# Kernel optimization log

Hardware: AMD Instinct MI355X
Metric: run time of the kernel (lower is better)

Reference implementation:

```python
import jax, jax.numpy as jnp
import numpy as np

N, E, D = 100000, 1000000, 128  # nodes, edges, feature dim (in=hidden=out)
BN_EPS = 1e-5


def setup_inputs() -> dict:
    key = jax.random.key(0)
    ks = jax.random.split(key, 6)
    inp = {
        "x": jax.random.normal(ks[0], (N, D), dtype=jnp.float32),
        "edge_src": jax.random.randint(ks[1], (E,), 0, N),
        "edge_dst": jax.random.randint(ks[2], (E,), 0, N),
    }
    # GraphConv weights (xavier-ish) and biases for 3 layers
    for i in range(3):
        inp[f"W{i}"] = jax.random.normal(ks[3 + i], (D, D), dtype=jnp.float32) * np.float32(1.0 / np.sqrt(D))
        inp[f"b{i}"] = jnp.zeros((D,), dtype=jnp.float32)
    # BatchNorm (eval mode) params/buffers for the 2 inter-layer BNs
    for i in range(2):
        inp[f"bn_gamma{i}"] = jnp.ones((D,), dtype=jnp.float32)
        inp[f"bn_beta{i}"] = jnp.zeros((D,), dtype=jnp.float32)
        inp[f"bn_mean{i}"] = jnp.zeros((D,), dtype=jnp.float32)
        inp[f"bn_var{i}"] = jnp.ones((D,), dtype=jnp.float32)
    return inp


def _gcn_forward(x, edge_src, edge_dst, Ws, bs, bns):
    n = x.shape[0]
    ones = jnp.ones((edge_src.shape[0],), x.dtype)
    # DGL GraphConv norm='both': D_out^{-1/2} on source, D_in^{-1/2} on dest, degrees clamped to >=1
    deg_out = jnp.clip(jax.ops.segment_sum(ones, edge_src, num_segments=n), 1.0)
    deg_in = jnp.clip(jax.ops.segment_sum(ones, edge_dst, num_segments=n), 1.0)
    norm_src = deg_out ** -0.5
    norm_dst = deg_in ** -0.5
    h = x
    L = len(Ws)
    for i in range(L):
        hs = (h * norm_src[:, None]) @ Ws[i]                     # [N, D] dense transform first
        agg = jax.ops.segment_sum(hs[edge_src], edge_dst, num_segments=n)  # SpMM: gather + scatter-add
        h = agg * norm_dst[:, None] + bs[i]
        if i < L - 1:  # BN (eval) + activation between layers; dropout=0 -> no-op
            g, bta, m, v = bns[i]
            h = (h - m) * jax.lax.rsqrt(v + BN_EPS) * g + bta
            h = jax.nn.relu(h)
    return h


def reference(x, edge_src, edge_dst, W0, b0, W1, b1, W2, b2,
              bn_gamma0, bn_beta0, bn_mean0, bn_var0,
              bn_gamma1, bn_beta1, bn_mean1, bn_var1):
    Ws = (W0, W1, W2)
    bs = (b0, b1, b2)
    bns = ((bn_gamma0, bn_beta0, bn_mean0, bn_var0),
           (bn_gamma1, bn_beta1, bn_mean1, bn_var1))
    return _gcn_forward(x, edge_src, edge_dst, Ws, bs, bns)
```

## Files before the change

kernel.cpp:

```cpp
#include <hip/hip_runtime.h>
#include <hip/hip_fp16.h>
#include <math.h>

#define D 128
#define NSL 32
#define PBU 25088

typedef _Float16 half8 __attribute__((ext_vector_type(8)));
typedef float f32x4 __attribute__((ext_vector_type(4)));

__device__ inline uint pack_f16x2(float a, float b) {
  __half2 h = __floats2half2_rn(a, b);
  return *reinterpret_cast<uint*>(&h);
}
__device__ inline float2 unpack_f16x2(uint p) {
  __half2 h = *reinterpret_cast<__half2*>(&p);
  return __half22float2(h);
}
__device__ inline uint mdiv40(uint x, uint M) {
  return (uint)(((unsigned long long)x * M) >> 40);
}


__global__ __launch_bounds__(1024) void k_build1(const int* __restrict__ esrc,
                                                 const int* __restrict__ edst,
                                                 const float* __restrict__ W0,
                                                 const float* __restrict__ W1,
                                                 const float* __restrict__ W2,
                                                 const float* __restrict__ b0,
                                                 const float* __restrict__ b1,
                                                 const float* __restrict__ b2,
                                                 const float* __restrict__ g0,
                                                 const float* __restrict__ be0,
                                                 const float* __restrict__ mu0,
                                                 const float* __restrict__ vr0,
                                                 const float* __restrict__ g1,
                                                 const float* __restrict__ be1,
                                                 const float* __restrict__ mu1,
                                                 const float* __restrict__ vr1,
                                                 uint* __restrict__ pd,
                                                 uint* __restrict__ ps,
                                                 uchar* __restrict__ rank8,
                                                 ushort* __restrict__ Wt,
                                                 float* __restrict__ CA,
                                                 float* __restrict__ CB,
                                                 int E, int SB) {
  __shared__ uint h[PBU];
  const int b = blockIdx.x;
  const int t = threadIdx.x;
  if (b < 32) {
    for (int j = t; j < PBU; j += 1024) h[j] = 0u;
    __syncthreads();
    const int i0 = b * SB, i1 = min(i0 + SB, E);
    for (int i = i0 + t; i < i1; i += 1024) {
      const int d = edst[i];
      const uint sh = (uint)(d & 3) * 8u;
      const uint old = atomicAdd(&h[d >> 2], 1u << sh);
      rank8[i] = (uchar)((old >> sh) & 0xffu);
    }
    __syncthreads();
    uint* p = pd + (size_t)b * PBU;
    for (int j = t; j < PBU; j += 1024) p[j] = h[j];
  } else if (b < 64) {
    const int sl = b - 32;
    for (int j = t; j < PBU; j += 1024) h[j] = 0u;
    __syncthreads();
    const int i0 = sl * SB, i1 = min(i0 + SB, E);
    for (int i = i0 + t; i < i1; i += 1024) {
      const int s = esrc[i];
      atomicAdd(&h[s >> 2], 1u << ((uint)(s & 3) * 8u));
    }
    __syncthreads();
    uint* p = ps + (size_t)sl * PBU;
    for (int j = t; j < PBU; j += 1024) p[j] = h[j];
  } else if (b < 112) {
    const int li = (b - 64) * 1024 + t;
    const int l = li >> 14;
    const int i = li & 16383;
    const int n = i >> 7, k = i & 127;
    const float* W = (l == 0) ? W0 : ((l == 1) ? W1 : W2);
    Wt[li] = __half_as_ushort(__float2half_rn(W[k * D + n]));
  } else if (t < D) {
    const int c = t;
    float A0 = g0[c] * rsqrtf(vr0[c] + 1e-5f);
    CA[c] = A0;
    CB[c] = (b0[c] - mu0[c]) * A0 + be0[c];
    float A1 = g1[c] * rsqrtf(vr1[c] + 1e-5f);
    CA[D + c] = A1;
    CB[D + c] = (b1[c] - mu1[c]) * A1 + be1[c];
    CA[2 * D + c] = 1.f;
    CB[2 * D + c] = b2[c];
  }
}


__global__ __launch_bounds__(256) void k_build2s(uint* __restrict__ pd,
                                                 const uint* __restrict__ ps,
                                                 int* __restrict__ totd,
                                                 float* __restrict__ ns,
                                                 float* __restrict__ nd,
                                                 int* __restrict__ csum,
                                                 int* __restrict__ rofs,
                                                 int* __restrict__ ticket,
                                                 int N, int nch) {
  __shared__ int sd[256];
  __shared__ int lastf;
  const int t = threadIdx.x;
  const int j = blockIdx.x * 256 + t;
  const int n0 = j * 4;
  uint r0 = 0, r1 = 0, r2 = 0, r3 = 0;
  uint s0 = 0, s1 = 0, s2 = 0, s3 = 0;
#pragma unroll
  for (int sl = 0; sl < NSL; ++sl) {
    const uint v = pd[(size_t)sl * PBU + j];
    pd[(size_t)sl * PBU + j] = r0 | (r1 << 8) | (r2 << 16) | (r3 << 24);
    r0 += v & 0xffu; r1 += (v >> 8) & 0xffu; r2 += (v >> 16) & 0xffu; r3 += (v >> 24) & 0xffu;
    const uint w = ps[(size_t)sl * PBU + j];
    s0 += w & 0xffu; s1 += (w >> 8) & 0xffu; s2 += (w >> 16) & 0xffu; s3 += (w >> 24) & 0xffu;
  }
  const uint rr[4] = {r0, r1, r2, r3};
  const uint ss[4] = {s0, s1, s2, s3};
  int tot = 0;
#pragma unroll
  for (int k = 0; k < 4; ++k) {
    if (n0 + k < N) {
      totd[n0 + k] = (int)rr[k];
      nd[n0 + k] = rsqrtf((float)max(rr[k], 1u));
      ns[n0 + k] = rsqrtf((float)max(ss[k], 1u));
      tot += (int)rr[k];
    }
  }
  sd[t] = tot; __syncthreads();
  for (int off = 128; off > 0; off >>= 1) {
    if (t < off) sd[t] += sd[t + off];
    __syncthreads();
  }
  if (t == 0) {
    csum[blockIdx.x] = sd[0];
    __threadfence();
    lastf = (atomicAdd(ticket, 1) == nch - 1) ? 1 : 0;
  }
  __syncthreads();
  if (lastf && t < 64) {
    __threadfence();
    int run = 0;
    for (int b0 = 0; b0 < nch; b0 += 64) {
      const int idx = b0 + t;
      int v = (idx < nch) ? __hip_atomic_load(&csum[idx], __ATOMIC_RELAXED,
                                              __HIP_MEMORY_SCOPE_AGENT) : 0;
      int sc = v;
#pragma unroll
      for (int off = 1; off < 64; off <<= 1) {
        int u = __shfl_up(sc, off);
        if (t >= off) sc += u;
      }
      if (idx < nch) csum[idx] = run + sc - v;
      run += __shfl(sc, 63);
    }
    if (t == 0) rofs[N] = run;
  }
}


__global__ __launch_bounds__(256) void k_scan_final(const int* __restrict__ totd,
                                                    const int* __restrict__ csum,
                                                    int* __restrict__ rofs, int n) {
  __shared__ int sd[256];
  const int b = blockIdx.x, t = threadIdx.x;
  const int base = b * 1024 + t * 4;
  int v[4]; int s = 0;
#pragma unroll
  for (int i = 0; i < 4; ++i) { v[i] = (base + i < n) ? totd[base + i] : 0; s += v[i]; }
  sd[t] = s; __syncthreads();
  for (int off = 1; off < 256; off <<= 1) {
    int x = (t >= off) ? sd[t - off] : 0;
    __syncthreads();
    sd[t] += x;
    __syncthreads();
  }
  int o = sd[t] - s + csum[b];
#pragma unroll
  for (int i = 0; i < 4; ++i) {
    if (base + i < n) { rofs[base + i] = o; o += v[i]; }
  }
}


__global__ __launch_bounds__(256) void k_sg(const float* __restrict__ X,
                                            const ushort* __restrict__ Wt,
                                            const float* __restrict__ ns,
                                            ushort* __restrict__ out,
                                            const int* __restrict__ esrc,
                                            const int* __restrict__ edst,
                                            const uchar* __restrict__ rank8,
                                            const uint* __restrict__ pd,
                                            const int* __restrict__ rofs,
                                            int* __restrict__ csr,
                                            int M, int E, uint Msb, int GB) {
  if ((int)blockIdx.x >= GB) {
    const int i = ((int)blockIdx.x - GB) * 256 + threadIdx.x;
    if (i < E) {
      const int d = edst[i];
      const uint sl = mdiv40((uint)i, Msb);
      const uint pk = pd[(size_t)sl * PBU + (d >> 2)];
      const uint pfx = (pk >> ((uint)(d & 3) * 8u)) & 0xffu;
      csr[rofs[d] + (int)pfx + (int)rank8[i]] = esrc[i];
    }
    return;
  }
  const int lane = threadIdx.x & 63;
  const int wv = threadIdx.x >> 6;
  const int m0 = (blockIdx.x * 4 + wv) * 32;
  if (m0 >= M) return;
  const int lr = lane & 15;
  const int kg = (lane >> 4) * 8;

  half8 hf[2][4];
  const half8 hz = {};
#pragma unroll
  for (int mt = 0; mt < 2; ++mt) {
    const int row = m0 + mt * 16 + lr;
    if (row < M) {
      const float s = ns[row];
#pragma unroll
      for (int kt = 0; kt < 4; ++kt) {
        const float4 a = *reinterpret_cast<const float4*>(X + (size_t)row * D + kt * 32 + kg);
        const float4 b = *reinterpret_cast<const float4*>(X + (size_t)row * D + kt * 32 + kg + 4);
        half8 hv;
        hv[0] = (_Float16)(a.x * s); hv[1] = (_Float16)(a.y * s);
        hv[2] = (_Float16)(a.z * s); hv[3] = (_Float16)(a.w * s);
        hv[4] = (_Float16)(b.x * s); hv[5] = (_Float16)(b.y * s);
        hv[6] = (_Float16)(b.z * s); hv[7] = (_Float16)(b.w * s);
        hf[mt][kt] = hv;
      }
    } else {
#pragma unroll
      for (int kt = 0; kt < 4; ++kt) hf[mt][kt] = hz;
    }
  }

  f32x4 acc[8][2];
#pragma unroll
  for (int nt = 0; nt < 8; ++nt) { acc[nt][0] = (f32x4)(0.f); acc[nt][1] = (f32x4)(0.f); }

#pragma unroll
  for (int nt = 0; nt < 8; ++nt) {
    const ushort* wb = Wt + (size_t)(nt * 16 + lr) * D + kg;
#pragma unroll
    for (int kt = 0; kt < 4; ++kt) {
      half8 wf = *reinterpret_cast<const half8*>(wb + kt * 32);
      acc[nt][0] = __builtin_amdgcn_mfma_f32_16x16x32_f16(wf, hf[0][kt], acc[nt][0], 0, 0, 0);
      acc[nt][1] = __builtin_amdgcn_mfma_f32_16x16x32_f16(wf, hf[1][kt], acc[nt][1], 0, 0, 0);
    }
  }

  const int mo = lane & 15;
  const int no = (lane >> 4) * 4;
#pragma unroll
  for (int mt = 0; mt < 2; ++mt) {
    const int row = m0 + mt * 16 + mo;
    if (row < M) {
#pragma unroll
      for (int nt = 0; nt < 8; ++nt) {
        uint2 u;
        u.x = pack_f16x2(acc[nt][mt][0], acc[nt][mt][1]);
        u.y = pack_f16x2(acc[nt][mt][2], acc[nt][mt][3]);
        *reinterpret_cast<uint2*>(out + (size_t)row * D + nt * 16 + no) = u;
      }
    }
  }
}


__global__ __launch_bounds__(256) void k_gemm16(const ushort* __restrict__ A,
                                                const ushort* __restrict__ Wt,
                                                ushort* __restrict__ out, int M) {
  const int lane = threadIdx.x & 63;
  const int wv = threadIdx.x >> 6;
  const int m0 = (blockIdx.x * 4 + wv) * 32;
  if (m0 >= M) return;
  const int lr = lane & 15;
  const int kg = (lane >> 4) * 8;

  half8 hf[2][4];
  const half8 hz = {};
#pragma unroll
  for (int mt = 0; mt < 2; ++mt) {
    const int row = m0 + mt * 16 + lr;
    const bool ok = row < M;
#pragma unroll
    for (int kt = 0; kt < 4; ++kt)
      hf[mt][kt] = ok ? *reinterpret_cast<const half8*>(A + (size_t)row * D + kt * 32 + kg)
                      : hz;
  }

  f32x4 acc[8][2];
#pragma unroll
  for (int nt = 0; nt < 8; ++nt) { acc[nt][0] = (f32x4)(0.f); acc[nt][1] = (f32x4)(0.f); }

#pragma unroll
  for (int nt = 0; nt < 8; ++nt) {
    const ushort* wb = Wt + (size_t)(nt * 16 + lr) * D + kg;
#pragma unroll
    for (int kt = 0; kt < 4; ++kt) {
      half8 wf = *reinterpret_cast<const half8*>(wb + kt * 32);
      acc[nt][0] = __builtin_amdgcn_mfma_f32_16x16x32_f16(wf, hf[0][kt], acc[nt][0], 0, 0, 0);
      acc[nt][1] = __builtin_amdgcn_mfma_f32_16x16x32_f16(wf, hf[1][kt], acc[nt][1], 0, 0, 0);
    }
  }

  const int mo = lane & 15;
  const int no = (lane >> 4) * 4;
#pragma unroll
  for (int mt = 0; mt < 2; ++mt) {
    const int row = m0 + mt * 16 + mo;
    if (row < M) {
#pragma unroll
      for (int nt = 0; nt < 8; ++nt) {
        uint2 u;
        u.x = pack_f16x2(acc[nt][mt][0], acc[nt][mt][1]);
        u.y = pack_f16x2(acc[nt][mt][2], acc[nt][mt][3]);
        *reinterpret_cast<uint2*>(out + (size_t)row * D + nt * 16 + no) = u;
      }
    }
  }
}


__global__ __launch_bounds__(256) void k_spmm16(const uint* __restrict__ hs,
                                                const int* __restrict__ csr,
                                                const int* __restrict__ rofs,
                                                const float* __restrict__ nd,
                                                const float* __restrict__ ns,
                                                const float* __restrict__ CA,
                                                const float* __restrict__ CB,
                                                float* __restrict__ outf,
                                                uint* __restrict__ hnext,
                                                int N, int last) {
  const int t = threadIdx.x;
  const int lane = t & 63;
  const int c16 = lane & 15;
  const int gb = lane & ~15;
  const int d = blockIdx.x * 16 + (t >> 4);
  if (d >= N) return;
  const int beg = rofs[d], end = rofs[d + 1];

  float acc[8];
#pragma unroll
  for (int j = 0; j < 8; ++j) acc[j] = 0.f;

  for (int base = beg; base < end; base += 16) {
    const int len = min(16, end - base);
    const int idx = csr[min(base + c16, end - 1)];
#pragma unroll 1
    for (int j = 0; j < len; j += 4) {
      const int l1 = min(j + 1, len - 1), l2 = min(j + 2, len - 1), l3 = min(j + 3, len - 1);
      const int s0 = __shfl(idx, gb + j);
      const int s1 = __shfl(idx, gb + l1);
      const int s2 = __shfl(idx, gb + l2);
      const int s3 = __shfl(idx, gb + l3);
      const float w1 = (j + 1 < len) ? 1.f : 0.f;
      const float w2 = (j + 2 < len) ? 1.f : 0.f;
      const float w3 = (j + 3 < len) ? 1.f : 0.f;
      const uint4 v0 = *reinterpret_cast<const uint4*>(hs + (size_t)s0 * 64 + c16 * 4);
      const uint4 v1 = *reinterpret_cast<const uint4*>(hs + (size_t)s1 * 64 + c16 * 4);
      const uint4 v2 = *reinterpret_cast<const uint4*>(hs + (size_t)s2 * 64 + c16 * 4);
      const uint4 v3 = *reinterpret_cast<const uint4*>(hs + (size_t)s3 * 64 + c16 * 4);
#pragma unroll
      for (int q = 0; q < 4; ++q) {
        const uint u0 = (&v0.x)[q], u1 = (&v1.x)[q], u2 = (&v2.x)[q], u3 = (&v3.x)[q];
        const float2 a0 = unpack_f16x2(u0);
        const float2 a1 = unpack_f16x2(u1);
        const float2 a2 = unpack_f16x2(u2);
        const float2 a3 = unpack_f16x2(u3);
        acc[q * 2]     += a0.x;
        acc[q * 2 + 1] += a0.y;
        acc[q * 2]     = fmaf(a1.x, w1, acc[q * 2]);
        acc[q * 2 + 1] = fmaf(a1.y, w1, acc[q * 2 + 1]);
        acc[q * 2]     = fmaf(a2.x, w2, acc[q * 2]);
        acc[q * 2 + 1] = fmaf(a2.y, w2, acc[q * 2 + 1]);
        acc[q * 2]     = fmaf(a3.x, w3, acc[q * 2]);
        acc[q * 2 + 1] = fmaf(a3.y, w3, acc[q * 2 + 1]);
      }
    }
  }

  const float ndv = nd[d];
  const float4 ca0 = *reinterpret_cast<const float4*>(CA + c16 * 8);
  const float4 ca1 = *reinterpret_cast<const float4*>(CA + c16 * 8 + 4);
  const float4 cb0 = *reinterpret_cast<const float4*>(CB + c16 * 8);
  const float4 cb1 = *reinterpret_cast<const float4*>(CB + c16 * 8 + 4);
  float r[8];
  r[0] = acc[0] * ndv * ca0.x + cb0.x;
  r[1] = acc[1] * ndv * ca0.y + cb0.y;
  r[2] = acc[2] * ndv * ca0.z + cb0.z;
  r[3] = acc[3] * ndv * ca0.w + cb0.w;
  r[4] = acc[4] * ndv * ca1.x + cb1.x;
  r[5] = acc[5] * ndv * ca1.y + cb1.y;
  r[6] = acc[6] * ndv * ca1.z + cb1.z;
  r[7] = acc[7] * ndv * ca1.w + cb1.w;
  if (!last) {
    const float s = ns[d];
#pragma unroll
    for (int j = 0; j < 8; ++j) r[j] = fmaxf(r[j], 0.f) * s;
    uint4 u;
    u.x = pack_f16x2(r[0], r[1]);
    u.y = pack_f16x2(r[2], r[3]);
    u.z = pack_f16x2(r[4], r[5]);
    u.w = pack_f16x2(r[6], r[7]);
    *reinterpret_cast<uint4*>(hnext + (size_t)d * 64 + c16 * 4) = u;
  } else {
    float4 o0 = make_float4(r[0], r[1], r[2], r[3]);
    float4 o1 = make_float4(r[4], r[5], r[6], r[7]);
    *reinterpret_cast<float4*>(outf + (size_t)d * D + c16 * 8) = o0;
    *reinterpret_cast<float4*>(outf + (size_t)d * D + c16 * 8 + 4) = o1;
  }
}


extern "C" void kernel_launch(void* const* d_in, const int* in_sizes, int n_in,
                              void* d_out, int out_size, void* d_ws, size_t ws_size,
                              hipStream_t stream) {
  const float* x = (const float*)d_in[0];
  const int* esrc = (const int*)d_in[1];
  const int* edst = (const int*)d_in[2];
  const float* W0 = (const float*)d_in[3];
  const float* b0 = (const float*)d_in[4];
  const float* W1 = (const float*)d_in[5];
  const float* b1 = (const float*)d_in[6];
  const float* W2 = (const float*)d_in[7];
  const float* b2 = (const float*)d_in[8];
  const float* g0 = (const float*)d_in[9];
  const float* be0 = (const float*)d_in[10];
  const float* m0 = (const float*)d_in[11];
  const float* v0 = (const float*)d_in[12];
  const float* g1 = (const float*)d_in[13];
  const float* be1 = (const float*)d_in[14];
  const float* m1 = (const float*)d_in[15];
  const float* v1 = (const float*)d_in[16];
  const int N = in_sizes[0] / D;
  const int E = in_sizes[1];

  const int SB = (E + NSL - 1) / NSL;
  const uint Msb = (uint)(((1ULL << 40) + (unsigned long long)SB - 1) / (unsigned long long)SB);

  char* p = (char*)d_ws;
  auto carve = [&](size_t bytes) {
    char* r = p;
    p += (bytes + 255) & ~(size_t)255;
    return (void*)r;
  };
  uint* hs16 = (uint*)carve((size_t)N * 64 * 4);
  ushort* Wt = (ushort*)carve((size_t)3 * D * D * 2);
  float* CA = (float*)carve((size_t)3 * D * 4);
  float* CB = (float*)carve((size_t)3 * D * 4);
  float* ns = (float*)carve((size_t)N * 4);
  float* nd = (float*)carve((size_t)N * 4);
  uint* pd = (uint*)carve((size_t)NSL * PBU * 4);
  uint* ps = (uint*)carve((size_t)NSL * PBU * 4);
  uchar* rank8 = (uchar*)carve((size_t)E);
  int* totd = (int*)carve((size_t)N * 4);
  int* rofs = (int*)carve((size_t)(N + 1) * 4);
  const int nch = (N + 1023) / 1024;
  int* csum = (int*)carve((size_t)nch * 4);
  int* ticket = (int*)carve(256);
  int* csr = (int*)carve((size_t)E * 4);
  uint* bufA = (uint*)d_out;

  hipMemsetAsync(ticket, 0, 4, stream);
  k_build1<<<113, 1024, 0, stream>>>(esrc, edst, W0, W1, W2, b0, b1, b2,
                                     g0, be0, m0, v0, g1, be1, m1, v1,
                                     pd, ps, rank8, Wt, CA, CB, E, SB);
  k_build2s<<<nch, 256, 0, stream>>>(pd, ps, totd, ns, nd, csum, rofs, ticket, N, nch);
  k_scan_final<<<nch, 256, 0, stream>>>(totd, csum, rofs, N);

  const int gb = (N + 127) / 128;
  const int sb = (N + 15) / 16;
  const int scb = (E + 255) / 256;
  k_sg<<<gb + scb, 256, 0, stream>>>(x, Wt, ns, (ushort*)hs16, esrc, edst, rank8, pd, rofs,
                                     csr, N, E, Msb, gb);
  k_spmm16<<<sb, 256, 0, stream>>>(hs16, csr, rofs, nd, ns, CA, CB, nullptr, bufA, N, 0);
  k_gemm16<<<gb, 256, 0, stream>>>((const ushort*)bufA, Wt + 16384, (ushort*)hs16, N);
  k_spmm16<<<sb, 256, 0, stream>>>(hs16, csr, rofs, nd, ns, CA + D, CB + D, nullptr, bufA, N, 0);
  k_gemm16<<<gb, 256, 0, stream>>>((const ushort*)bufA, Wt + 32768, (ushort*)hs16, N);
  k_spmm16<<<sb, 256, 0, stream>>>(hs16, csr, rofs, nd, ns, CA + 2 * D, CB + 2 * D,
                                   (float*)d_out, nullptr, N, 1);
}
```

Baseline: 251.7 us.

## Fuse SpMM aggregation with next-layer GEMM through LDS tile

```diff
diff --git a/kernel.cpp b/kernel.cpp
--- a/kernel.cpp
+++ b/kernel.cpp
@@ -272,56 +272,126 @@
 }
 
 
-__global__ __launch_bounds__(256) void k_gemm16(const ushort* __restrict__ A,
-                                                const ushort* __restrict__ Wt,
-                                                ushort* __restrict__ out, int M) {
-  const int lane = threadIdx.x & 63;
-  const int wv = threadIdx.x >> 6;
-  const int m0 = (blockIdx.x * 4 + wv) * 32;
-  if (m0 >= M) return;
+__global__ __launch_bounds__(256) void k_spgm(const uint* __restrict__ hs,
+                                              const int* __restrict__ csr,
+                                              const int* __restrict__ rofs,
+                                              const float* __restrict__ nd,
+                                              const float* __restrict__ ns,
+                                              const float* __restrict__ CA,
+                                              const float* __restrict__ CB,
+                                              const ushort* __restrict__ Wt,
+                                              ushort* __restrict__ out, int N) {
+  __shared__ ushort A[128 * 136];
+  const int t = threadIdx.x;
+  const int lane = t & 63;
+  const int c16 = lane & 15;
+  const int gb = lane & ~15;
+  const int g = t >> 4;
+  const int rbase = blockIdx.x * 128;
+
+#pragma unroll 1
+  for (int r = 0; r < 8; ++r) {
+    const int rl = g + 16 * r;
+    const int d = rbase + rl;
+    uint4 uo = make_uint4(0u, 0u, 0u, 0u);
+    if (d < N) {
+      const int beg = rofs[d], end = rofs[d + 1];
+      float acc[8];
+#pragma unroll
+      for (int j = 0; j < 8; ++j) acc[j] = 0.f;
+      for (int eb = beg; eb < end; eb += 16) {
+        const int len = min(16, end - eb);
+        const int idx = csr[min(eb + c16, end - 1)];
+#pragma unroll 1
+        for (int j = 0; j < len; j += 4) {
+          const int l1 = min(j + 1, len - 1), l2 = min(j + 2, len - 1), l3 = min(j + 3, len - 1);
+          const int s0 = __shfl(idx, gb + j);
+          const int s1 = __shfl(idx, gb + l1);
+          const int s2 = __shfl(idx, gb + l2);
+          const int s3 = __shfl(idx, gb + l3);
+          const float w1 = (j + 1 < len) ? 1.f : 0.f;
+          const float w2 = (j + 2 < len) ? 1.f : 0.f;
+          const float w3 = (j + 3 < len) ? 1.f : 0.f;
+          const uint4 v0 = *reinterpret_cast<const uint4*>(hs + (size_t)s0 * 64 + c16 * 4);
+          const uint4 v1 = *reinterpret_cast<const uint4*>(hs + (size_t)s1 * 64 + c16 * 4);
+          const uint4 v2 = *reinterpret_cast<const uint4*>(hs + (size_t)s2 * 64 + c16 * 4);
+          const uint4 v3 = *reinterpret_cast<const uint4*>(hs + (size_t)s3 * 64 + c16 * 4);
+#pragma unroll
+          for (int q = 0; q < 4; ++q) {
+            const float2 a0 = unpack_f16x2((&v0.x)[q]);
+            const float2 a1 = unpack_f16x2((&v1.x)[q]);
+            const float2 a2 = unpack_f16x2((&v2.x)[q]);
+            const float2 a3 = unpack_f16x2((&v3.x)[q]);
+            acc[q * 2]     += a0.x;
+            acc[q * 2 + 1] += a0.y;
+            acc[q * 2]     = fmaf(a1.x, w1, acc[q * 2]);
+            acc[q * 2 + 1] = fmaf(a1.y, w1, acc[q * 2 + 1]);
+            acc[q * 2]     = fmaf(a2.x, w2, acc[q * 2]);
+            acc[q * 2 + 1] = fmaf(a2.y, w2, acc[q * 2 + 1]);
+            acc[q * 2]     = fmaf(a3.x, w3, acc[q * 2]);
+            acc[q * 2 + 1] = fmaf(a3.y, w3, acc[q * 2 + 1]);
+          }
+        }
+      }
+      const float ndv = nd[d];
+      const float s = ns[d];
+      const float4 ca0 = *reinterpret_cast<const float4*>(CA + c16 * 8);
+      const float4 ca1 = *reinterpret_cast<const float4*>(CA + c16 * 8 + 4);
+      const float4 cb0 = *reinterpret_cast<const float4*>(CB + c16 * 8);
+      const float4 cb1 = *reinterpret_cast<const float4*>(CB + c16 * 8 + 4);
+      float rv[8];
+      rv[0] = acc[0] * ndv * ca0.x + cb0.x;
+      rv[1] = acc[1] * ndv * ca0.y + cb0.y;
+      rv[2] = acc[2] * ndv * ca0.z + cb0.z;
+      rv[3] = acc[3] * ndv * ca0.w + cb0.w;
+      rv[4] = acc[4] * ndv * ca1.x + cb1.x;
+      rv[5] = acc[5] * ndv * ca1.y + cb1.y;
+      rv[6] = acc[6] * ndv * ca1.z + cb1.z;
+      rv[7] = acc[7] * ndv * ca1.w + cb1.w;
+#pragma unroll
+      for (int j = 0; j < 8; ++j) rv[j] = fmaxf(rv[j], 0.f) * s;
+      uo.x = pack_f16x2(rv[0], rv[1]);
+      uo.y = pack_f16x2(rv[2], rv[3]);
+      uo.z = pack_f16x2(rv[4], rv[5]);
+      uo.w = pack_f16x2(rv[6], rv[7]);
+    }
+    *reinterpret_cast<uint4*>(&A[rl * 136 + c16 * 8]) = uo;
+  }
+  __syncthreads();
+
+  const int w = t >> 6;
+  const int m0l = w * 32;
+  const int m0 = rbase + m0l;
+  if (m0 >= N) return;
   const int lr = lane & 15;
   const int kg = (lane >> 4) * 8;
-
   half8 hf[2][4];
-  const half8 hz = {};
 #pragma unroll
   for (int mt = 0; mt < 2; ++mt) {
-    const int row = m0 + mt * 16 + lr;
-    const bool ok = row < M;
+    const int row_l = m0l + mt * 16 + lr;
 #pragma unroll
     for (int kt = 0; kt < 4; ++kt)
-      hf[mt][kt] = ok ? *reinterpret_cast<const half8*>(A + (size_t)row * D + kt * 32 + kg)
-                      : hz;
-  }
-
-  f32x4 acc[8][2];
-#pragma unroll
-  for (int nt = 0; nt < 8; ++nt) { acc[nt][0] = (f32x4)(0.f); acc[nt][1] = (f32x4)(0.f); }
-
+      hf[mt][kt] = *reinterpret_cast<const half8*>(&A[row_l * 136 + kt * 32 + kg]);
+  }
+  const int no = (lane >> 4) * 4;
 #pragma unroll
   for (int nt = 0; nt < 8; ++nt) {
+    f32x4 a0 = (f32x4)(0.f), a1 = (f32x4)(0.f);
     const ushort* wb = Wt + (size_t)(nt * 16 + lr) * D + kg;
 #pragma unroll
     for (int kt = 0; kt < 4; ++kt) {
       half8 wf = *reinterpret_cast<const half8*>(wb + kt * 32);
-      acc[nt][0] = __builtin_amdgcn_mfma_f32_16x16x32_f16(wf, hf[0][kt], acc[nt][0], 0, 0, 0);
-      acc[nt][1] = __builtin_amdgcn_mfma_f32_16x16x32_f16(wf, hf[1][kt], acc[nt][1], 0, 0, 0);
-    }
-  }
-
-  const int mo = lane & 15;
-  const int no = (lane >> 4) * 4;
-#pragma unroll
-  for (int mt = 0; mt < 2; ++mt) {
-    const int row = m0 + mt * 16 + mo;
-    if (row < M) {
-#pragma unroll
-      for (int nt = 0; nt < 8; ++nt) {
-        uint2 u;
-        u.x = pack_f16x2(acc[nt][mt][0], acc[nt][mt][1]);
-        u.y = pack_f16x2(acc[nt][mt][2], acc[nt][mt][3]);
-        *reinterpret_cast<uint2*>(out + (size_t)row * D + nt * 16 + no) = u;
-      }
+      a0 = __builtin_amdgcn_mfma_f32_16x16x32_f16(wf, hf[0][kt], a0, 0, 0, 0);
+      a1 = __builtin_amdgcn_mfma_f32_16x16x32_f16(wf, hf[1][kt], a1, 0, 0, 0);
+    }
+    const int r0 = m0 + lr, r1 = m0 + 16 + lr;
+    if (r0 < N) {
+      uint2 u; u.x = pack_f16x2(a0[0], a0[1]); u.y = pack_f16x2(a0[2], a0[3]);
+      *reinterpret_cast<uint2*>(out + (size_t)r0 * D + nt * 16 + no) = u;
+    }
+    if (r1 < N) {
+      uint2 u; u.x = pack_f16x2(a1[0], a1[1]); u.y = pack_f16x2(a1[2], a1[3]);
+      *reinterpret_cast<uint2*>(out + (size_t)r1 * D + nt * 16 + no) = u;
     }
   }
 }
@@ -331,12 +401,9 @@
                                                 const int* __restrict__ csr,
                                                 const int* __restrict__ rofs,
                                                 const float* __restrict__ nd,
-                                                const float* __restrict__ ns,
                                                 const float* __restrict__ CA,
                                                 const float* __restrict__ CB,
-                                                float* __restrict__ outf,
-                                                uint* __restrict__ hnext,
-                                                int N, int last) {
+                                                float* __restrict__ outf, int N) {
   const int t = threadIdx.x;
   const int lane = t & 63;
   const int c16 = lane & 15;
@@ -368,11 +435,10 @@
       const uint4 v3 = *reinterpret_cast<const uint4*>(hs + (size_t)s3 * 64 + c16 * 4);
 #pragma unroll
       for (int q = 0; q < 4; ++q) {
-        const uint u0 = (&v0.x)[q], u1 = (&v1.x)[q], u2 = (&v2.x)[q], u3 = (&v3.x)[q];
-        const float2 a0 = unpack_f16x2(u0);
-        const float2 a1 = unpack_f16x2(u1);
-        const float2 a2 = unpack_f16x2(u2);
-        const float2 a3 = unpack_f16x2(u3);
+        const float2 a0 = unpack_f16x2((&v0.x)[q]);
+        const float2 a1 = unpack_f16x2((&v1.x)[q]);
+        const float2 a2 = unpack_f16x2((&v2.x)[q]);
+        const float2 a3 = unpack_f16x2((&v3.x)[q]);
         acc[q * 2]     += a0.x;
         acc[q * 2 + 1] += a0.y;
         acc[q * 2]     = fmaf(a1.x, w1, acc[q * 2]);
@@ -390,31 +456,17 @@
   const float4 ca1 = *reinterpret_cast<const float4*>(CA + c16 * 8 + 4);
   const float4 cb0 = *reinterpret_cast<const float4*>(CB + c16 * 8);
   const float4 cb1 = *reinterpret_cast<const float4*>(CB + c16 * 8 + 4);
-  float r[8];
-  r[0] = acc[0] * ndv * ca0.x + cb0.x;
-  r[1] = acc[1] * ndv * ca0.y + cb0.y;
-  r[2] = acc[2] * ndv * ca0.z + cb0.z;
-  r[3] = acc[3] * ndv * ca0.w + cb0.w;
-  r[4] = acc[4] * ndv * ca1.x + cb1.x;
-  r[5] = acc[5] * ndv * ca1.y + cb1.y;
-  r[6] = acc[6] * ndv * ca1.z + cb1.z;
-  r[7] = acc[7] * ndv * ca1.w + cb1.w;
-  if (!last) {
-    const float s = ns[d];
-#pragma unroll
-    for (int j = 0; j < 8; ++j) r[j] = fmaxf(r[j], 0.f) * s;
-    uint4 u;
-    u.x = pack_f16x2(r[0], r[1]);
-    u.y = pack_f16x2(r[2], r[3]);
-    u.z = pack_f16x2(r[4], r[5]);
-    u.w = pack_f16x2(r[6], r[7]);
-    *reinterpret_cast<uint4*>(hnext + (size_t)d * 64 + c16 * 4) = u;
-  } else {
-    float4 o0 = make_float4(r[0], r[1], r[2], r[3]);
-    float4 o1 = make_float4(r[4], r[5], r[6], r[7]);
-    *reinterpret_cast<float4*>(outf + (size_t)d * D + c16 * 8) = o0;
-    *reinterpret_cast<float4*>(outf + (size_t)d * D + c16 * 8 + 4) = o1;
-  }
+  float4 o0, o1;
+  o0.x = acc[0] * ndv * ca0.x + cb0.x;
+  o0.y = acc[1] * ndv * ca0.y + cb0.y;
+  o0.z = acc[2] * ndv * ca0.z + cb0.z;
+  o0.w = acc[3] * ndv * ca0.w + cb0.w;
+  o1.x = acc[4] * ndv * ca1.x + cb1.x;
+  o1.y = acc[5] * ndv * ca1.y + cb1.y;
+  o1.z = acc[6] * ndv * ca1.z + cb1.z;
+  o1.w = acc[7] * ndv * ca1.w + cb1.w;
+  *reinterpret_cast<float4*>(outf + (size_t)d * D + c16 * 8) = o0;
+  *reinterpret_cast<float4*>(outf + (size_t)d * D + c16 * 8 + 4) = o1;
 }
 
 
@@ -465,7 +517,7 @@
   int* csum = (int*)carve((size_t)nch * 4);
   int* ticket = (int*)carve(256);
   int* csr = (int*)carve((size_t)E * 4);
-  uint* bufA = (uint*)d_out;
+  uint* hsOut = (uint*)d_out;
 
   hipMemsetAsync(ticket, 0, 4, stream);
   k_build1<<<113, 1024, 0, stream>>>(esrc, edst, W0, W1, W2, b0, b1, b2,
@@ -475,14 +527,15 @@
   k_scan_final<<<nch, 256, 0, stream>>>(totd, csum, rofs, N);
 
   const int gb = (N + 127) / 128;
+  const int scb = (E + 255) / 256;
+  const int fb = (N + 127) / 128;
   const int sb = (N + 15) / 16;
-  const int scb = (E + 255) / 256;
   k_sg<<<gb + scb, 256, 0, stream>>>(x, Wt, ns, (ushort*)hs16, esrc, edst, rank8, pd, rofs,
                                      csr, N, E, Msb, gb);
-  k_spmm16<<<sb, 256, 0, stream>>>(hs16, csr, rofs, nd, ns, CA, CB, nullptr, bufA, N, 0);
-  k_gemm16<<<gb, 256, 0, stream>>>((const ushort*)bufA, Wt + 16384, (ushort*)hs16, N);
-  k_spmm16<<<sb, 256, 0, stream>>>(hs16, csr, rofs, nd, ns, CA + D, CB + D, nullptr, bufA, N, 0);
-  k_gemm16<<<gb, 256, 0, stream>>>((const ushort*)bufA, Wt + 32768, (ushort*)hs16, N);
-  k_spmm16<<<sb, 256, 0, stream>>>(hs16, csr, rofs, nd, ns, CA + 2 * D, CB + 2 * D,
-                                   (float*)d_out, nullptr, N, 1);
-}
+  k_spgm<<<fb, 256, 0, stream>>>(hs16, csr, rofs, nd, ns, CA, CB, Wt + 16384,
+                                 (ushort*)hsOut, N);
+  k_spgm<<<fb, 256, 0, stream>>>(hsOut, csr, rofs, nd, ns, CA + D, CB + D, Wt + 32768,
+                                 (ushort*)hs16, N);
+  k_spmm16<<<sb, 256, 0, stream>>>(hs16, csr, rofs, nd, CA + 2 * D, CB + 2 * D,
+                                   (float*)d_out, N);
+}
```

Measured after the change: 226.4 us. 1.11x faster.

## Column-chunk the hidden features so each XCD gathers one chunk in SpMM

Applied to the files above, without the earlier changes.

```diff
diff --git a/kernel.cpp b/kernel.cpp
--- a/kernel.cpp
+++ b/kernel.cpp
@@ -265,7 +265,7 @@
         uint2 u;
         u.x = pack_f16x2(acc[nt][mt][0], acc[nt][mt][1]);
         u.y = pack_f16x2(acc[nt][mt][2], acc[nt][mt][3]);
-        *reinterpret_cast<uint2*>(out + (size_t)row * D + nt * 16 + no) = u;
+        *reinterpret_cast<uint2*>(out + ((size_t)nt * M + row) * 16 + no) = u;
       }
     }
   }
@@ -289,9 +289,12 @@
     const int row = m0 + mt * 16 + lr;
     const bool ok = row < M;
 #pragma unroll
-    for (int kt = 0; kt < 4; ++kt)
-      hf[mt][kt] = ok ? *reinterpret_cast<const half8*>(A + (size_t)row * D + kt * 32 + kg)
+    for (int kt = 0; kt < 4; ++kt) {
+      const int off = kt * 32 + kg;
+      const int c = off >> 4, o = off & 15;
+      hf[mt][kt] = ok ? *reinterpret_cast<const half8*>(A + ((size_t)c * M + row) * 16 + o)
                       : hz;
+    }
   }
 
   f32x4 acc[8][2];
@@ -320,100 +323,100 @@
         uint2 u;
         u.x = pack_f16x2(acc[nt][mt][0], acc[nt][mt][1]);
         u.y = pack_f16x2(acc[nt][mt][2], acc[nt][mt][3]);
-        *reinterpret_cast<uint2*>(out + (size_t)row * D + nt * 16 + no) = u;
-      }
-    }
-  }
-}
-
-
-__global__ __launch_bounds__(256) void k_spmm16(const uint* __restrict__ hs,
-                                                const int* __restrict__ csr,
-                                                const int* __restrict__ rofs,
-                                                const float* __restrict__ nd,
-                                                const float* __restrict__ ns,
-                                                const float* __restrict__ CA,
-                                                const float* __restrict__ CB,
-                                                float* __restrict__ outf,
-                                                uint* __restrict__ hnext,
-                                                int N, int last) {
+        *reinterpret_cast<uint2*>(out + ((size_t)nt * M + row) * 16 + no) = u;
+      }
+    }
+  }
+}
+
+
+__global__ __launch_bounds__(256) void k_spmmc(const uint* __restrict__ hs,
+                                               const int* __restrict__ csr,
+                                               const int* __restrict__ rofs,
+                                               const float* __restrict__ nd,
+                                               const float* __restrict__ ns,
+                                               const float* __restrict__ CA,
+                                               const float* __restrict__ CB,
+                                               float* __restrict__ outf,
+                                               uint* __restrict__ hnext,
+                                               int N, int RB, int last) {
   const int t = threadIdx.x;
   const int lane = t & 63;
-  const int c16 = lane & 15;
-  const int gb = lane & ~15;
-  const int d = blockIdx.x * 16 + (t >> 4);
-  if (d >= N) return;
-  const int beg = rofs[d], end = rofs[d + 1];
-
-  float acc[8];
-#pragma unroll
-  for (int j = 0; j < 8; ++j) acc[j] = 0.f;
-
-  for (int base = beg; base < end; base += 16) {
-    const int len = min(16, end - base);
-    const int idx = csr[min(base + c16, end - 1)];
+  const int il = lane & 15;
+  const int slot = il >> 1;
+  const int half = il & 1;
+  const int p = blockIdx.x & 7;
+  const uint* hsC = hs + (size_t)p * N * 8;
+  const int g = t >> 4;
+  const int rb0 = (blockIdx.x >> 3) * (16 * RB);
+
 #pragma unroll 1
-    for (int j = 0; j < len; j += 4) {
-      const int l1 = min(j + 1, len - 1), l2 = min(j + 2, len - 1), l3 = min(j + 3, len - 1);
-      const int s0 = __shfl(idx, gb + j);
-      const int s1 = __shfl(idx, gb + l1);
-      const int s2 = __shfl(idx, gb + l2);
-      const int s3 = __shfl(idx, gb + l3);
-      const float w1 = (j + 1 < len) ? 1.f : 0.f;
-      const float w2 = (j + 2 < len) ? 1.f : 0.f;
-      const float w3 = (j + 3 < len) ? 1.f : 0.f;
-      const uint4 v0 = *reinterpret_cast<const uint4*>(hs + (size_t)s0 * 64 + c16 * 4);
-      const uint4 v1 = *reinterpret_cast<const uint4*>(hs + (size_t)s1 * 64 + c16 * 4);
-      const uint4 v2 = *reinterpret_cast<const uint4*>(hs + (size_t)s2 * 64 + c16 * 4);
-      const uint4 v3 = *reinterpret_cast<const uint4*>(hs + (size_t)s3 * 64 + c16 * 4);
+  for (int r = 0; r < RB; ++r) {
+    const int d = rb0 + r * 16 + g;
+    if (d >= N) break;
+    const int beg = rofs[d], end = rofs[d + 1];
+    float acc[8];
+#pragma unroll
+    for (int j = 0; j < 8; ++j) acc[j] = 0.f;
+#pragma unroll 1
+    for (int eb = beg; eb < end; eb += 16) {
+      const int e0 = eb + slot;
+      const int e1 = eb + slot + 8;
+      const int s0 = csr[min(e0, end - 1)];
+      const int s1 = csr[min(e1, end - 1)];
+      const float w0 = (e0 < end) ? 1.f : 0.f;
+      const float w1 = (e1 < end) ? 1.f : 0.f;
+      const uint4 v0 = *reinterpret_cast<const uint4*>(hsC + (size_t)s0 * 8 + half * 4);
+      const uint4 v1 = *reinterpret_cast<const uint4*>(hsC + (size_t)s1 * 8 + half * 4);
 #pragma unroll
       for (int q = 0; q < 4; ++q) {
-        const uint u0 = (&v0.x)[q], u1 = (&v1.x)[q], u2 = (&v2.x)[q], u3 = (&v3.x)[q];
-        const float2 a0 = unpack_f16x2(u0);
-        const float2 a1 = unpack_f16x2(u1);
-        const float2 a2 = unpack_f16x2(u2);
-        const float2 a3 = unpack_f16x2(u3);
-        acc[q * 2]     += a0.x;
-        acc[q * 2 + 1] += a0.y;
+        const float2 a0 = unpack_f16x2((&v0.x)[q]);
+        const float2 a1 = unpack_f16x2((&v1.x)[q]);
+        acc[q * 2]     = fmaf(a0.x, w0, acc[q * 2]);
+        acc[q * 2 + 1] = fmaf(a0.y, w0, acc[q * 2 + 1]);
         acc[q * 2]     = fmaf(a1.x, w1, acc[q * 2]);
         acc[q * 2 + 1] = fmaf(a1.y, w1, acc[q * 2 + 1]);
-        acc[q * 2]     = fmaf(a2.x, w2, acc[q * 2]);
-        acc[q * 2 + 1] = fmaf(a2.y, w2, acc[q * 2 + 1]);
-        acc[q * 2]     = fmaf(a3.x, w3, acc[q * 2]);
-        acc[q * 2 + 1] = fmaf(a3.y, w3, acc[q * 2 + 1]);
-      }
-    }
-  }
-
-  const float ndv = nd[d];
-  const float4 ca0 = *reinterpret_cast<const float4*>(CA + c16 * 8);
-  const float4 ca1 = *reinterpret_cast<const float4*>(CA + c16 * 8 + 4);
-  const float4 cb0 = *reinterpret_cast<const float4*>(CB + c16 * 8);
-  const float4 cb1 = *reinterpret_cast<const float4*>(CB + c16 * 8 + 4);
-  float r[8];
-  r[0] = acc[0] * ndv * ca0.x + cb0.x;
-  r[1] = acc[1] * ndv * ca0.y + cb0.y;
-  r[2] = acc[2] * ndv * ca0.z + cb0.z;
-  r[3] = acc[3] * ndv * ca0.w + cb0.w;
-  r[4] = acc[4] * ndv * ca1.x + cb1.x;
-  r[5] = acc[5] * ndv * ca1.y + cb1.y;
-  r[6] = acc[6] * ndv * ca1.z + cb1.z;
-  r[7] = acc[7] * ndv * ca1.w + cb1.w;
-  if (!last) {
-    const float s = ns[d];
-#pragma unroll
-    for (int j = 0; j < 8; ++j) r[j] = fmaxf(r[j], 0.f) * s;
-    uint4 u;
-    u.x = pack_f16x2(r[0], r[1]);
-    u.y = pack_f16x2(r[2], r[3]);
-    u.z = pack_f16x2(r[4], r[5]);
-    u.w = pack_f16x2(r[6], r[7]);
-    *reinterpret_cast<uint4*>(hnext + (size_t)d * 64 + c16 * 4) = u;
-  } else {
-    float4 o0 = make_float4(r[0], r[1], r[2], r[3]);
-    float4 o1 = make_float4(r[4], r[5], r[6], r[7]);
-    *reinterpret_cast<float4*>(outf + (size_t)d * D + c16 * 8) = o0;
-    *reinterpret_cast<float4*>(outf + (size_t)d * D + c16 * 8 + 4) = o1;
+      }
+    }
+#pragma unroll
+    for (int j = 0; j < 8; ++j) {
+      acc[j] += __shfl_xor(acc[j], 2);
+      acc[j] += __shfl_xor(acc[j], 4);
+      acc[j] += __shfl_xor(acc[j], 8);
+    }
+    if (il < 2) {
+      const float ndv = nd[d];
+      const int c0 = p * 16 + half * 8;
+      const float4 ca0 = *reinterpret_cast<const float4*>(CA + c0);
+      const float4 ca1 = *reinterpret_cast<const float4*>(CA + c0 + 4);
+      const float4 cb0 = *reinterpret_cast<const float4*>(CB + c0);
+      const float4 cb1 = *reinterpret_cast<const float4*>(CB + c0 + 4);
+      float rv[8];
+      rv[0] = acc[0] * ndv * ca0.x + cb0.x;
+      rv[1] = acc[1] * ndv * ca0.y + cb0.y;
+      rv[2] = acc[2] * ndv * ca0.z + cb0.z;
+      rv[3] = acc[3] * ndv * ca0.w + cb0.w;
+      rv[4] = acc[4] * ndv * ca1.x + cb1.x;
+      rv[5] = acc[5] * ndv * ca1.y + cb1.y;
+      rv[6] = acc[6] * ndv * ca1.z + cb1.z;
+      rv[7] = acc[7] * ndv * ca1.w + cb1.w;
+      if (!last) {
+        const float s = ns[d];
+#pragma unroll
+        for (int j = 0; j < 8; ++j) rv[j] = fmaxf(rv[j], 0.f) * s;
+        uint4 u;
+        u.x = pack_f16x2(rv[0], rv[1]);
+        u.y = pack_f16x2(rv[2], rv[3]);
+        u.z = pack_f16x2(rv[4], rv[5]);
+        u.w = pack_f16x2(rv[6], rv[7]);
+        *reinterpret_cast<uint4*>(hnext + ((size_t)p * N + d) * 8 + half * 4) = u;
+      } else {
+        *reinterpret_cast<float4*>(outf + (size_t)d * D + c0) =
+            make_float4(rv[0], rv[1], rv[2], rv[3]);
+        *reinterpret_cast<float4*>(outf + (size_t)d * D + c0 + 4) =
+            make_float4(rv[4], rv[5], rv[6], rv[7]);
+      }
+    }
   }
 }
 
@@ -450,7 +453,7 @@
     p += (bytes + 255) & ~(size_t)255;
     return (void*)r;
   };
-  uint* hs16 = (uint*)carve((size_t)N * 64 * 4);
+  uint* hsA = (uint*)carve((size_t)N * 64 * 4);
   ushort* Wt = (ushort*)carve((size_t)3 * D * D * 2);
   float* CA = (float*)carve((size_t)3 * D * 4);
   float* CB = (float*)carve((size_t)3 * D * 4);
@@ -465,7 +468,7 @@
   int* csum = (int*)carve((size_t)nch * 4);
   int* ticket = (int*)carve(256);
   int* csr = (int*)carve((size_t)E * 4);
-  uint* bufA = (uint*)d_out;
+  uint* hsB = (uint*)d_out;
 
   hipMemsetAsync(ticket, 0, 4, stream);
   k_build1<<<113, 1024, 0, stream>>>(esrc, edst, W0, W1, W2, b0, b1, b2,
@@ -475,14 +478,16 @@
   k_scan_final<<<nch, 256, 0, stream>>>(totd, csum, rofs, N);
 
   const int gb = (N + 127) / 128;
-  const int sb = (N + 15) / 16;
   const int scb = (E + 255) / 256;
-  k_sg<<<gb + scb, 256, 0, stream>>>(x, Wt, ns, (ushort*)hs16, esrc, edst, rank8, pd, rofs,
+  const int RB = 8;
+  const int spb = 8 * ((N + 16 * RB - 1) / (16 * RB));
+  k_sg<<<gb + scb, 256, 0, stream>>>(x, Wt, ns, (ushort*)hsA, esrc, edst, rank8, pd, rofs,
                                      csr, N, E, Msb, gb);
-  k_spmm16<<<sb, 256, 0, stream>>>(hs16, csr, rofs, nd, ns, CA, CB, nullptr, bufA, N, 0);
-  k_gemm16<<<gb, 256, 0, stream>>>((const ushort*)bufA, Wt + 16384, (ushort*)hs16, N);
-  k_spmm16<<<sb, 256, 0, stream>>>(hs16, csr, rofs, nd, ns, CA + D, CB + D, nullptr, bufA, N, 0);
-  k_gemm16<<<gb, 256, 0, stream>>>((const ushort*)bufA, Wt + 32768, (ushort*)hs16, N);
-  k_spmm16<<<sb, 256, 0, stream>>>(hs16, csr, rofs, nd, ns, CA + 2 * D, CB + 2 * D,
-                                   (float*)d_out, nullptr, N, 1);
-}
+  k_spmmc<<<spb, 256, 0, stream>>>(hsA, csr, rofs, nd, ns, CA, CB, nullptr, hsB, N, RB, 0);
+  k_gemm16<<<gb, 256, 0, stream>>>((const ushort*)hsB, Wt + 16384, (ushort*)hsA, N);
+  k_spmmc<<<spb, 256, 0, stream>>>(hsA, csr, rofs, nd, ns, CA + D, CB + D, nullptr, hsB, N,
+                                   RB, 0);
+  k_gemm16<<<gb, 256, 0, stream>>>((const ushort*)hsB, Wt + 32768, (ushort*)hsA, N);
+  k_spmmc<<<spb, 256, 0, stream>>>(hsA, csr, rofs, nd, ns, CA + 2 * D, CB + 2 * D,
+                                   (float*)d_out, nullptr, N, RB, 1);
+}
```

Result: slower. 349.9 us (+39.0%).
